# Kernel tuning notes

Hardware: AMD Instinct MI355X
Metric: run time of the kernel (lower is better)

The kernel has to match this reference:

```python
import jax, jax.numpy as jnp
import numpy as np

N, T, K, C, O = 2048, 20, 32, 32, 64  # agents, timesteps, neighbors, in_ch, out_ch


def setup_inputs() -> dict:
    key = jax.random.key(0)
    ks = jax.random.split(key, 8)
    s = 0.05
    x = jax.random.normal(ks[0], (N, T, C), dtype=jnp.float32)
    A = jax.random.randint(ks[1], (T, N, K), 0, N)  # neighbor indices into agent dim
    conv_w = jax.random.normal(ks[2], (O, C), jnp.float32) * s  # 1x1 conv == linear [O,C]
    conv_b = jax.random.normal(ks[3], (O,), jnp.float32) * s
    w_ih = jax.random.normal(ks[4], (4 * O, O), jnp.float32) * s  # LSTM gates i,f,g,o
    w_hh = jax.random.normal(ks[5], (4 * O, O), jnp.float32) * s
    b_ih = jax.random.normal(ks[6], (4 * O,), jnp.float32) * s
    b_hh = jax.random.normal(ks[7], (4 * O,), jnp.float32) * s
    return dict(x=x, A=A, conv_w=conv_w, conv_b=conv_b,
                w_ih=w_ih, w_hh=w_hh, b_ih=b_ih, b_hh=b_hh)


def reference(x, A, conv_w, conv_b, w_ih, w_hh, b_ih, b_hh):
    n = x.shape[0]
    xt = jnp.transpose(x, (1, 0, 2))  # [T, N, C]
    # align == 1: per-timestep neighbor gather and relative difference
    gathered = jax.vmap(lambda xs, idx: xs[idx])(xt, A)  # [T, N, K, C]
    diff = gathered - xt[:, :, None, :]  # [T, N, K, C]
    # 1x1 conv (pointwise linear over channels)
    y = jnp.einsum('tnkc,oc->tnko', diff, conv_w) + conv_b  # [T, N, K, O]
    # AdaptiveMaxPool2d((seq_len, 1)): max over the neighbor axis K
    feat = jnp.max(y, axis=2)  # [T, N, O] -- LSTM input (time-major)

    h0 = jnp.zeros((n, O), jnp.float32)
    c0 = jnp.zeros((n, O), jnp.float32)

    def step(carry, x_t):
        h, c = carry
        g = x_t @ w_ih.T + h @ w_hh.T + (b_ih + b_hh)  # [N, 4O]
        i_g, f_g, g_g, o_g = jnp.split(g, 4, axis=-1)
        c = jax.nn.sigmoid(f_g) * c + jax.nn.sigmoid(i_g) * jnp.tanh(g_g)
        h = jax.nn.sigmoid(o_g) * jnp.tanh(c)
        return (h, c), h

    (hN, cN), hs = jax.lax.scan(step, (h0, c0), feat)
    out = jnp.transpose(hs, (1, 0, 2))  # [N, T, O]
    # state_tuple permuted to batch-first as in the torch module
    return out, hN[:, None, :], cN[:, None, :]
```

## Files before the change

kernel.cpp:

```cpp
#include <hip/hip_runtime.h>
#include <hip/hip_bf16.h>
#include <math.h>

#define NA 2048
#define TT 20
#define KK 32
#define CC 32
#define OO 64
#define GG 256
#define SW 88

typedef __attribute__((ext_vector_type(8))) short short8;
typedef __attribute__((ext_vector_type(4))) float float4v;
typedef __attribute__((ext_vector_type(4))) unsigned uint4v;

__device__ __forceinline__ float fast_rcp(float x) {
    return __builtin_amdgcn_rcpf(x);
}
__device__ __forceinline__ float sigm(float x) {
    return fast_rcp(1.f + __expf(-x));
}
__device__ __forceinline__ float tanh_fast(float x) {
    return 1.f - 2.f * fast_rcp(1.f + __expf(2.f * x));
}
__device__ __forceinline__ short f2bs(float f) {
    __hip_bfloat16 h = __float2bfloat16(f);
    short s;
    __builtin_memcpy(&s, &h, 2);
    return s;
}
__device__ __forceinline__ float bf_lo(unsigned u) {
    return __uint_as_float(u << 16);
}
__device__ __forceinline__ float bf_hi(unsigned u) {
    return __uint_as_float(u & 0xffff0000u);
}
__device__ __forceinline__ unsigned pack2(float a, float b) {
    return (unsigned)(unsigned short)f2bs(a) | ((unsigned)(unsigned short)f2bs(b) << 16);
}

__global__ __launch_bounds__(256) void proj_kernel(
    const float* __restrict__ x, const float* __restrict__ conv_w,
    __hip_bfloat16* __restrict__ P)
{
    const int lane = threadIdx.x & 63;
    const int wv = threadIdx.x >> 6;
    float w[CC];
    #pragma unroll
    for (int c = 0; c < CC; c += 4) {
        float4 v = *(const float4*)(conv_w + lane * CC + c);
        w[c] = v.x; w[c + 1] = v.y; w[c + 2] = v.z; w[c + 3] = v.w;
    }
    const int rbase = blockIdx.x * 16 + wv * 4;
    #pragma unroll
    for (int i = 0; i < 4; ++i) {
        int r = rbase + i;
        const float* xr = x + (size_t)r * CC;
        float a0 = 0.f, a1 = 0.f;
        #pragma unroll
        for (int c = 0; c < CC; c += 8) {
            float4 v = *(const float4*)(xr + c);
            float4 u = *(const float4*)(xr + c + 4);
            a0 = fmaf(v.x, w[c], a0);     a0 = fmaf(v.y, w[c + 1], a0);
            a0 = fmaf(v.z, w[c + 2], a0); a0 = fmaf(v.w, w[c + 3], a0);
            a1 = fmaf(u.x, w[c + 4], a1); a1 = fmaf(u.y, w[c + 5], a1);
            a1 = fmaf(u.z, w[c + 6], a1); a1 = fmaf(u.w, w[c + 7], a1);
        }
        int n = r / TT;
        int t = r - n * TT;
        P[(((size_t)t << 11) + n) * OO + lane] = __float2bfloat16(a0 + a1);
    }
}

__global__ __launch_bounds__(256, 3) void gatemm_kernel(
    const __hip_bfloat16* __restrict__ P, const int* __restrict__ A,
    const float* __restrict__ conv_b, const float* __restrict__ w_ih,
    const float* __restrict__ b_ih, const float* __restrict__ b_hh,
    __hip_bfloat16* __restrict__ gx)
{
    const int tid = threadIdx.x;
    const int lane = tid & 63;
    const int wv = tid >> 6;
    const int l15 = lane & 15;
    const int q = lane >> 4;

    const int bs = (blockIdx.x & 7) * 320 + (blockIdx.x >> 3);
    const int r0 = bs << 4;
    const int t = r0 >> 11;
    const int n0 = r0 & (NA - 1);
    const unsigned short* Pb = (const unsigned short*)P + ((size_t)t << 17);

    __shared__ float bias_sh[GG];
    __shared__ __align__(16) unsigned short feat_sh[16 * SW];

    {
        float bj = b_ih[tid] + b_hh[tid];
        #pragma unroll
        for (int o = 0; o < OO; o += 4) {
            float4 cb = *(const float4*)(conv_b + o);
            float4 wr = *(const float4*)(w_ih + (size_t)tid * OO + o);
            bj = fmaf(cb.x, wr.x, bj); bj = fmaf(cb.y, wr.y, bj);
            bj = fmaf(cb.z, wr.z, bj); bj = fmaf(cb.w, wr.w, bj);
        }
        bias_sh[tid] = bj;
    }

    const int i_row = lane >> 4;
    const int ko2   = (lane >> 3) & 1;
    const int oc    = lane & 7;

    const int myrow = r0 + wv * 4 + i_row;
    const int* aRow = A + ((size_t)myrow << 5) + ko2;

    int ai[16];
    #pragma unroll
    for (int g = 0; g < 16; ++g) ai[g] = aRow[g * 2];
    uint4v sv = *(const uint4v*)(Pb + ((size_t)(n0 + wv * 4 + i_row) << 6) + oc * 8);
    asm volatile("" ::: "memory");

    uint4v pv[16];
    #pragma unroll
    for (int g = 0; g < 16; ++g)
        pv[g] = *(const uint4v*)(Pb + ((size_t)ai[g] << 6) + oc * 8);
    asm volatile("" ::: "memory");

    float mx[8];
    #pragma unroll
    for (int e = 0; e < 8; ++e) mx[e] = -INFINITY;
    #pragma unroll
    for (int g = 0; g < 16; ++g) {
        uint4v v = pv[g];
        mx[0] = fmaxf(mx[0], bf_lo(v[0])); mx[1] = fmaxf(mx[1], bf_hi(v[0]));
        mx[2] = fmaxf(mx[2], bf_lo(v[1])); mx[3] = fmaxf(mx[3], bf_hi(v[1]));
        mx[4] = fmaxf(mx[4], bf_lo(v[2])); mx[5] = fmaxf(mx[5], bf_hi(v[2]));
        mx[6] = fmaxf(mx[6], bf_lo(v[3])); mx[7] = fmaxf(mx[7], bf_hi(v[3]));
    }
    #pragma unroll
    for (int e = 0; e < 8; ++e)
        mx[e] = fmaxf(mx[e], __shfl_xor(mx[e], 8, 64));

    if (ko2 == 0) {
        uint4v pk;
        pk[0] = pack2(mx[0] - bf_lo(sv[0]), mx[1] - bf_hi(sv[0]));
        pk[1] = pack2(mx[2] - bf_lo(sv[1]), mx[3] - bf_hi(sv[1]));
        pk[2] = pack2(mx[4] - bf_lo(sv[2]), mx[5] - bf_hi(sv[2]));
        pk[3] = pack2(mx[6] - bf_lo(sv[3]), mx[7] - bf_hi(sv[3]));
        *(uint4v*)&feat_sh[(wv * 4 + i_row) * SW + oc * 8] = pk;
    }
    __syncthreads();

    short8 bfrag[4][2];
    #pragma unroll
    for (int tt2 = 0; tt2 < 4; ++tt2) {
        int j = wv * 64 + tt2 * 16 + l15;
        #pragma unroll
        for (int ks = 0; ks < 2; ++ks) {
            int k0 = ks * 32 + q * 8;
            float4 w0 = *(const float4*)(w_ih + (size_t)j * OO + k0);
            float4 w1 = *(const float4*)(w_ih + (size_t)j * OO + k0 + 4);
            short8 bf;
            bf[0] = f2bs(w0.x); bf[1] = f2bs(w0.y);
            bf[2] = f2bs(w0.z); bf[3] = f2bs(w0.w);
            bf[4] = f2bs(w1.x); bf[5] = f2bs(w1.y);
            bf[6] = f2bs(w1.z); bf[7] = f2bs(w1.w);
            bfrag[tt2][ks] = bf;
        }
    }

    float4v acc[4] = {{0.f, 0.f, 0.f, 0.f}, {0.f, 0.f, 0.f, 0.f},
                      {0.f, 0.f, 0.f, 0.f}, {0.f, 0.f, 0.f, 0.f}};
    #pragma unroll
    for (int ks = 0; ks < 2; ++ks) {
        short8 af = *(const short8*)(&feat_sh[l15 * SW + ks * 32 + q * 8]);
        #pragma unroll
        for (int tt2 = 0; tt2 < 4; ++tt2)
            acc[tt2] = __builtin_amdgcn_mfma_f32_16x16x32_bf16(
                af, bfrag[tt2][ks], acc[tt2], 0, 0, 0);
    }

    #pragma unroll
    for (int tt2 = 0; tt2 < 4; ++tt2) {
        int j = wv * 64 + tt2 * 16 + l15;
        float bv = bias_sh[j];
        #pragma unroll
        for (int rg = 0; rg < 4; ++rg)
            gx[((size_t)(r0 + q * 4 + rg) << 8) + j] =
                __float2bfloat16(acc[tt2][rg] + bv);
    }
}

__global__ __launch_bounds__(256, 4) void lstm_kernel(
    const __hip_bfloat16* __restrict__ gx, const float* __restrict__ w_hh,
    float* __restrict__ out)
{
    const int tid = threadIdx.x;
    const int lane = tid & 63;
    const int wv = tid >> 6;
    const int l15 = lane & 15;
    const int q = lane >> 4;
    const int a0 = blockIdx.x * 16;
    const int a = tid >> 4;
    const int c0 = (tid & 15) * 4;

    short8 bfrag[4][2];
    #pragma unroll
    for (int tt2 = 0; tt2 < 4; ++tt2) {
        int row = wv * 64 + tt2 * 16 + l15;
        #pragma unroll
        for (int ks = 0; ks < 2; ++ks) {
            int k0 = ks * 32 + q * 8;
            float4 w0 = *(const float4*)(w_hh + (size_t)row * OO + k0);
            float4 w1 = *(const float4*)(w_hh + (size_t)row * OO + k0 + 4);
            short8 bf;
            bf[0] = f2bs(w0.x); bf[1] = f2bs(w0.y);
            bf[2] = f2bs(w0.z); bf[3] = f2bs(w0.w);
            bf[4] = f2bs(w1.x); bf[5] = f2bs(w1.y);
            bf[6] = f2bs(w1.z); bf[7] = f2bs(w1.w);
            bfrag[tt2][ks] = bf;
        }
    }

    __shared__ __align__(16) unsigned short h_sh[16 * 72];
    __shared__ float gp[4][16][68];

    {
        uint2 z; z.x = 0u; z.y = 0u;
        *(uint2*)&h_sh[a * 72 + c0] = z;
    }
    float cst[4] = {0.f, 0.f, 0.f, 0.f};

    const unsigned short* gxp = (const unsigned short*)gx;
    uint2 gxv[4];
    #pragma unroll
    for (int g = 0; g < 4; ++g)
        gxv[g] = *(const uint2*)(gxp + ((size_t)(a0 + a) << 8) + g * 64 + c0);

    for (int t = 0; t < TT; ++t) {
        __syncthreads();

        float4v acc[4] = {{0.f, 0.f, 0.f, 0.f}, {0.f, 0.f, 0.f, 0.f},
                          {0.f, 0.f, 0.f, 0.f}, {0.f, 0.f, 0.f, 0.f}};
        #pragma unroll
        for (int ks = 0; ks < 2; ++ks) {
            short8 af = *(const short8*)(&h_sh[l15 * 72 + ks * 32 + q * 8]);
            #pragma unroll
            for (int tt2 = 0; tt2 < 4; ++tt2)
                acc[tt2] = __builtin_amdgcn_mfma_f32_16x16x32_bf16(
                    af, bfrag[tt2][ks], acc[tt2], 0, 0, 0);
        }
        #pragma unroll
        for (int tt2 = 0; tt2 < 4; ++tt2)
            #pragma unroll
            for (int rg = 0; rg < 4; ++rg)
                gp[wv][q * 4 + rg][tt2 * 16 + l15] = acc[tt2][rg];

        uint2 gxn[4];
        int tn = (t + 1 < TT) ? t + 1 : t;
        #pragma unroll
        for (int g = 0; g < 4; ++g)
            gxn[g] = *(const uint2*)(gxp + (((size_t)tn << 11) + a0 + a) * GG
                                     + g * 64 + c0);
        __syncthreads();

        float4 gv0 = *(const float4*)&gp[0][a][c0];
        float4 gv1 = *(const float4*)&gp[1][a][c0];
        float4 gv2 = *(const float4*)&gp[2][a][c0];
        float4 gv3 = *(const float4*)&gp[3][a][c0];
        float hv[4];
        {
            float gi[4] = {gv0.x + bf_lo(gxv[0].x), gv0.y + bf_hi(gxv[0].x),
                           gv0.z + bf_lo(gxv[0].y), gv0.w + bf_hi(gxv[0].y)};
            float gf[4] = {gv1.x + bf_lo(gxv[1].x), gv1.y + bf_hi(gxv[1].x),
                           gv1.z + bf_lo(gxv[1].y), gv1.w + bf_hi(gxv[1].y)};
            float gz[4] = {gv2.x + bf_lo(gxv[2].x), gv2.y + bf_hi(gxv[2].x),
                           gv2.z + bf_lo(gxv[2].y), gv2.w + bf_hi(gxv[2].y)};
            float go[4] = {gv3.x + bf_lo(gxv[3].x), gv3.y + bf_hi(gxv[3].x),
                           gv3.z + bf_lo(gxv[3].y), gv3.w + bf_hi(gxv[3].y)};
            #pragma unroll
            for (int e = 0; e < 4; ++e) {
                float ig = sigm(gi[e]);
                float fg = sigm(gf[e]);
                float zg = tanh_fast(gz[e]);
                float og = sigm(go[e]);
                cst[e] = fmaf(fg, cst[e], ig * zg);
                hv[e] = og * tanh_fast(cst[e]);
            }
        }
        {
            uint2 pk;
            pk.x = pack2(hv[0], hv[1]);
            pk.y = pack2(hv[2], hv[3]);
            *(uint2*)&h_sh[a * 72 + c0] = pk;
        }
        float4 ho; ho.x = hv[0]; ho.y = hv[1]; ho.z = hv[2]; ho.w = hv[3];
        *(float4*)(out + (((size_t)(a0 + a) * TT + t) << 6) + c0) = ho;
        if (t == TT - 1) {
            size_t hb = (size_t)NA * TT * OO;
            *(float4*)(out + hb + ((size_t)(a0 + a) << 6) + c0) = ho;
            float4 co; co.x = cst[0]; co.y = cst[1]; co.z = cst[2]; co.w = cst[3];
            *(float4*)(out + hb + ((size_t)NA << 6) + ((size_t)(a0 + a) << 6) + c0) = co;
        }
        gxv[0] = gxn[0]; gxv[1] = gxn[1]; gxv[2] = gxn[2]; gxv[3] = gxn[3];
    }
}

extern "C" void kernel_launch(void* const* d_in, const int* in_sizes, int n_in,
                              void* d_out, int out_size, void* d_ws, size_t ws_size,
                              hipStream_t stream) {
    const float* x      = (const float*)d_in[0];
    const int*   A      = (const int*)  d_in[1];
    const float* conv_w = (const float*)d_in[2];
    const float* conv_b = (const float*)d_in[3];
    const float* w_ih   = (const float*)d_in[4];
    const float* w_hh   = (const float*)d_in[5];
    const float* b_ih   = (const float*)d_in[6];
    const float* b_hh   = (const float*)d_in[7];
    float* out = (float*)d_out;

    __hip_bfloat16* P = (__hip_bfloat16*)d_ws;
    __hip_bfloat16* gx =
        (__hip_bfloat16*)((char*)d_ws + (size_t)TT * NA * OO * sizeof(__hip_bfloat16));

    hipLaunchKernelGGL(proj_kernel, dim3(NA * TT / 16), dim3(256), 0, stream,
                       x, conv_w, P);
    hipLaunchKernelGGL(gatemm_kernel, dim3(NA * TT / 16), dim3(256), 0, stream,
                       P, A, conv_b, w_ih, b_ih, b_hh, gx);
    hipLaunchKernelGGL(lstm_kernel, dim3(NA / 16), dim3(256), 0, stream,
                       gx, w_hh, out);
}
```

Measured before the change: 157.3 us.

## Precompute bf16 weights and fused bias once, stage gate outputs, halve LSTM block agents

```diff
diff --git a/kernel.cpp b/kernel.cpp
--- a/kernel.cpp
+++ b/kernel.cpp
@@ -9,6 +9,7 @@
 #define OO 64
 #define GG 256
 #define SW 88
+#define GXP 264
 
 typedef __attribute__((ext_vector_type(8))) short short8;
 typedef __attribute__((ext_vector_type(4))) float float4v;
@@ -23,11 +24,12 @@
 __device__ __forceinline__ float tanh_fast(float x) {
     return 1.f - 2.f * fast_rcp(1.f + __expf(2.f * x));
 }
-__device__ __forceinline__ short f2bs(float f) {
-    __hip_bfloat16 h = __float2bfloat16(f);
-    short s;
-    __builtin_memcpy(&s, &h, 2);
-    return s;
+__device__ __forceinline__ unsigned cvt_rne(float f) {
+    unsigned u = __float_as_uint(f);
+    return (u + 0x7FFFu + ((u >> 16) & 1u)) >> 16;
+}
+__device__ __forceinline__ unsigned pack2(float a, float b) {
+    return cvt_rne(a) | (cvt_rne(b) << 16);
 }
 __device__ __forceinline__ float bf_lo(unsigned u) {
     return __uint_as_float(u << 16);
@@ -35,23 +37,41 @@
 __device__ __forceinline__ float bf_hi(unsigned u) {
     return __uint_as_float(u & 0xffff0000u);
 }
-__device__ __forceinline__ unsigned pack2(float a, float b) {
-    return (unsigned)(unsigned short)f2bs(a) | ((unsigned)(unsigned short)f2bs(b) << 16);
-}
 
 __global__ __launch_bounds__(256) void proj_kernel(
     const float* __restrict__ x, const float* __restrict__ conv_w,
-    __hip_bfloat16* __restrict__ P)
+    const float* __restrict__ conv_b, const float* __restrict__ w_ih,
+    const float* __restrict__ w_hh, const float* __restrict__ b_ih,
+    const float* __restrict__ b_hh,
+    __hip_bfloat16* __restrict__ P, unsigned short* __restrict__ wihb,
+    unsigned short* __restrict__ whhb, float* __restrict__ biasT)
 {
-    const int lane = threadIdx.x & 63;
-    const int wv = threadIdx.x >> 6;
+    const int tid = threadIdx.x;
+    if (blockIdx.x == 0) {
+        for (int e = tid; e < 4 * OO * OO; e += 256) {
+            wihb[e] = (unsigned short)cvt_rne(w_ih[e]);
+            whhb[e] = (unsigned short)cvt_rne(w_hh[e]);
+        }
+        float bj = b_ih[tid] + b_hh[tid];
+        #pragma unroll
+        for (int o = 0; o < OO; o += 4) {
+            float4 cb = *(const float4*)(conv_b + o);
+            float4 wr = *(const float4*)(w_ih + (size_t)tid * OO + o);
+            bj = fmaf(cb.x, wr.x, bj); bj = fmaf(cb.y, wr.y, bj);
+            bj = fmaf(cb.z, wr.z, bj); bj = fmaf(cb.w, wr.w, bj);
+        }
+        biasT[tid] = bj;
+        return;
+    }
+    const int lane = tid & 63;
+    const int wv = tid >> 6;
     float w[CC];
     #pragma unroll
     for (int c = 0; c < CC; c += 4) {
         float4 v = *(const float4*)(conv_w + lane * CC + c);
         w[c] = v.x; w[c + 1] = v.y; w[c + 2] = v.z; w[c + 3] = v.w;
     }
-    const int rbase = blockIdx.x * 16 + wv * 4;
+    const int rbase = (blockIdx.x - 1) * 16 + wv * 4;
     #pragma unroll
     for (int i = 0; i < 4; ++i) {
         int r = rbase + i;
@@ -68,14 +88,14 @@
         }
         int n = r / TT;
         int t = r - n * TT;
-        P[(((size_t)t << 11) + n) * OO + lane] = __float2bfloat16(a0 + a1);
-    }
-}
-
-__global__ __launch_bounds__(256, 3) void gatemm_kernel(
+        ((unsigned short*)P)[(((size_t)t << 11) + n) * OO + lane] =
+            (unsigned short)cvt_rne(a0 + a1);
+    }
+}
+
+__global__ __launch_bounds__(256, 6) void gatemm_kernel(
     const __hip_bfloat16* __restrict__ P, const int* __restrict__ A,
-    const float* __restrict__ conv_b, const float* __restrict__ w_ih,
-    const float* __restrict__ b_ih, const float* __restrict__ b_hh,
+    const unsigned short* __restrict__ wihb, const float* __restrict__ biasT,
     __hip_bfloat16* __restrict__ gx)
 {
     const int tid = threadIdx.x;
@@ -90,19 +110,22 @@
     const int n0 = r0 & (NA - 1);
     const unsigned short* Pb = (const unsigned short*)P + ((size_t)t << 17);
 
-    __shared__ float bias_sh[GG];
     __shared__ __align__(16) unsigned short feat_sh[16 * SW];
-
-    {
-        float bj = b_ih[tid] + b_hh[tid];
-        #pragma unroll
-        for (int o = 0; o < OO; o += 4) {
-            float4 cb = *(const float4*)(conv_b + o);
-            float4 wr = *(const float4*)(w_ih + (size_t)tid * OO + o);
-            bj = fmaf(cb.x, wr.x, bj); bj = fmaf(cb.y, wr.y, bj);
-            bj = fmaf(cb.z, wr.z, bj); bj = fmaf(cb.w, wr.w, bj);
-        }
-        bias_sh[tid] = bj;
+    __shared__ __align__(16) unsigned short gx_sh[16 * GXP];
+
+    float bv[4];
+    #pragma unroll
+    for (int tt2 = 0; tt2 < 4; ++tt2)
+        bv[tt2] = biasT[wv * 64 + tt2 * 16 + l15];
+
+    short8 bfrag[4][2];
+    #pragma unroll
+    for (int tt2 = 0; tt2 < 4; ++tt2) {
+        int j = wv * 64 + tt2 * 16 + l15;
+        #pragma unroll
+        for (int ks = 0; ks < 2; ++ks)
+            bfrag[tt2][ks] =
+                *(const short8*)(wihb + ((size_t)j << 6) + ks * 32 + q * 8);
     }
 
     const int i_row = lane >> 4;
@@ -149,24 +172,6 @@
     }
     __syncthreads();
 
-    short8 bfrag[4][2];
-    #pragma unroll
-    for (int tt2 = 0; tt2 < 4; ++tt2) {
-        int j = wv * 64 + tt2 * 16 + l15;
-        #pragma unroll
-        for (int ks = 0; ks < 2; ++ks) {
-            int k0 = ks * 32 + q * 8;
-            float4 w0 = *(const float4*)(w_ih + (size_t)j * OO + k0);
-            float4 w1 = *(const float4*)(w_ih + (size_t)j * OO + k0 + 4);
-            short8 bf;
-            bf[0] = f2bs(w0.x); bf[1] = f2bs(w0.y);
-            bf[2] = f2bs(w0.z); bf[3] = f2bs(w0.w);
-            bf[4] = f2bs(w1.x); bf[5] = f2bs(w1.y);
-            bf[6] = f2bs(w1.z); bf[7] = f2bs(w1.w);
-            bfrag[tt2][ks] = bf;
-        }
-    }
-
     float4v acc[4] = {{0.f, 0.f, 0.f, 0.f}, {0.f, 0.f, 0.f, 0.f},
                       {0.f, 0.f, 0.f, 0.f}, {0.f, 0.f, 0.f, 0.f}};
     #pragma unroll
@@ -181,16 +186,25 @@
     #pragma unroll
     for (int tt2 = 0; tt2 < 4; ++tt2) {
         int j = wv * 64 + tt2 * 16 + l15;
-        float bv = bias_sh[j];
         #pragma unroll
         for (int rg = 0; rg < 4; ++rg)
-            gx[((size_t)(r0 + q * 4 + rg) << 8) + j] =
-                __float2bfloat16(acc[tt2][rg] + bv);
-    }
-}
-
-__global__ __launch_bounds__(256, 4) void lstm_kernel(
-    const __hip_bfloat16* __restrict__ gx, const float* __restrict__ w_hh,
+            gx_sh[(q * 4 + rg) * GXP + j] =
+                (unsigned short)cvt_rne(acc[tt2][rg] + bv[tt2]);
+    }
+    __syncthreads();
+    {
+        const int m = tid >> 4;
+        const int j0 = (tid & 15) * 16;
+        uint4v d0 = *(const uint4v*)&gx_sh[m * GXP + j0];
+        uint4v d1 = *(const uint4v*)&gx_sh[m * GXP + j0 + 8];
+        unsigned short* gp_out = (unsigned short*)gx + ((size_t)(r0 + m) << 8) + j0;
+        *(uint4v*)gp_out = d0;
+        *(uint4v*)(gp_out + 8) = d1;
+    }
+}
+
+__global__ __launch_bounds__(256, 2) void lstm_kernel(
+    const __hip_bfloat16* __restrict__ gx, const unsigned short* __restrict__ whhb,
     float* __restrict__ out)
 {
     const int tid = threadIdx.x;
@@ -198,26 +212,19 @@
     const int wv = tid >> 6;
     const int l15 = lane & 15;
     const int q = lane >> 4;
-    const int a0 = blockIdx.x * 16;
+    const int a0 = blockIdx.x * 8;
     const int a = tid >> 4;
     const int c0 = (tid & 15) * 4;
+    const int ag = (a < 8) ? (a0 + a) : (NA - 1);
 
     short8 bfrag[4][2];
     #pragma unroll
     for (int tt2 = 0; tt2 < 4; ++tt2) {
         int row = wv * 64 + tt2 * 16 + l15;
         #pragma unroll
-        for (int ks = 0; ks < 2; ++ks) {
-            int k0 = ks * 32 + q * 8;
-            float4 w0 = *(const float4*)(w_hh + (size_t)row * OO + k0);
-            float4 w1 = *(const float4*)(w_hh + (size_t)row * OO + k0 + 4);
-            short8 bf;
-            bf[0] = f2bs(w0.x); bf[1] = f2bs(w0.y);
-            bf[2] = f2bs(w0.z); bf[3] = f2bs(w0.w);
-            bf[4] = f2bs(w1.x); bf[5] = f2bs(w1.y);
-            bf[6] = f2bs(w1.z); bf[7] = f2bs(w1.w);
-            bfrag[tt2][ks] = bf;
-        }
+        for (int ks = 0; ks < 2; ++ks)
+            bfrag[tt2][ks] =
+                *(const short8*)(whhb + ((size_t)row << 6) + ks * 32 + q * 8);
     }
 
     __shared__ __align__(16) unsigned short h_sh[16 * 72];
@@ -233,7 +240,7 @@
     uint2 gxv[4];
     #pragma unroll
     for (int g = 0; g < 4; ++g)
-        gxv[g] = *(const uint2*)(gxp + ((size_t)(a0 + a) << 8) + g * 64 + c0);
+        gxv[g] = *(const uint2*)(gxp + ((size_t)ag << 8) + g * 64 + c0);
 
     for (int t = 0; t < TT; ++t) {
         __syncthreads();
@@ -258,7 +265,7 @@
         int tn = (t + 1 < TT) ? t + 1 : t;
         #pragma unroll
         for (int g = 0; g < 4; ++g)
-            gxn[g] = *(const uint2*)(gxp + (((size_t)tn << 11) + a0 + a) * GG
+            gxn[g] = *(const uint2*)(gxp + (((size_t)tn << 11) + ag) * GG
                                      + g * 64 + c0);
         __syncthreads();
 
@@ -288,17 +295,21 @@
         }
         {
             uint2 pk;
-            pk.x = pack2(hv[0], hv[1]);
-            pk.y = pack2(hv[2], hv[3]);
+            if (a < 8) {
+                pk.x = pack2(hv[0], hv[1]);
+                pk.y = pack2(hv[2], hv[3]);
+            } else { pk.x = 0u; pk.y = 0u; }
             *(uint2*)&h_sh[a * 72 + c0] = pk;
         }
-        float4 ho; ho.x = hv[0]; ho.y = hv[1]; ho.z = hv[2]; ho.w = hv[3];
-        *(float4*)(out + (((size_t)(a0 + a) * TT + t) << 6) + c0) = ho;
-        if (t == TT - 1) {
-            size_t hb = (size_t)NA * TT * OO;
-            *(float4*)(out + hb + ((size_t)(a0 + a) << 6) + c0) = ho;
-            float4 co; co.x = cst[0]; co.y = cst[1]; co.z = cst[2]; co.w = cst[3];
-            *(float4*)(out + hb + ((size_t)NA << 6) + ((size_t)(a0 + a) << 6) + c0) = co;
+        if (a < 8) {
+            float4 ho; ho.x = hv[0]; ho.y = hv[1]; ho.z = hv[2]; ho.w = hv[3];
+            *(float4*)(out + (((size_t)ag * TT + t) << 6) + c0) = ho;
+            if (t == TT - 1) {
+                size_t hb = (size_t)NA * TT * OO;
+                *(float4*)(out + hb + ((size_t)ag << 6) + c0) = ho;
+                float4 co; co.x = cst[0]; co.y = cst[1]; co.z = cst[2]; co.w = cst[3];
+                *(float4*)(out + hb + ((size_t)NA << 6) + ((size_t)ag << 6) + c0) = co;
+            }
         }
         gxv[0] = gxn[0]; gxv[1] = gxn[1]; gxv[2] = gxn[2]; gxv[3] = gxn[3];
     }
@@ -317,14 +328,20 @@
     const float* b_hh   = (const float*)d_in[7];
     float* out = (float*)d_out;
 
-    __hip_bfloat16* P = (__hip_bfloat16*)d_ws;
-    __hip_bfloat16* gx =
-        (__hip_bfloat16*)((char*)d_ws + (size_t)TT * NA * OO * sizeof(__hip_bfloat16));
-
-    hipLaunchKernelGGL(proj_kernel, dim3(NA * TT / 16), dim3(256), 0, stream,
-                       x, conv_w, P);
+    char* ws = (char*)d_ws;
+    __hip_bfloat16* P  = (__hip_bfloat16*)ws;
+    size_t offGx = (size_t)TT * NA * OO * 2;
+    __hip_bfloat16* gx = (__hip_bfloat16*)(ws + offGx);
+    size_t offW  = offGx + (size_t)TT * NA * GG * 2;
+    unsigned short* wihb = (unsigned short*)(ws + offW);
+    unsigned short* whhb = wihb + 4 * OO * OO;
+    float* biasT = (float*)(whhb + 4 * OO * OO);
+
+    hipLaunchKernelGGL(proj_kernel, dim3(NA * TT / 16 + 1), dim3(256), 0, stream,
+                       x, conv_w, conv_b, w_ih, w_hh, b_ih, b_hh,
+                       P, wihb, whhb, biasT);
     hipLaunchKernelGGL(gatemm_kernel, dim3(NA * TT / 16), dim3(256), 0, stream,
-                       P, A, conv_b, w_ih, b_ih, b_hh, gx);
-    hipLaunchKernelGGL(lstm_kernel, dim3(NA / 16), dim3(256), 0, stream,
-                       gx, w_hh, out);
-}
+                       P, A, wihb, biasT, gx);
+    hipLaunchKernelGGL(lstm_kernel, dim3(NA / 8), dim3(256), 0, stream,
+                       gx, whhb, out);
+}
```

Result: slower. 164.1 us (+4.3%).
